# Performance work log

Hardware: AMD Instinct MI355X
Metric: run time of the kernel (lower is better)

## Reference

```python
import jax, jax.numpy as jnp
import numpy as np

EPS = 1e-12


def setup_inputs() -> dict:
    key = jax.random.key(0)
    n, k, Eu, iterations = 200_000, 7, 1_600_000, 3
    k1, k2, k3 = jax.random.split(key, 3)
    # undirected edge list; each undirected edge yields two directed edges
    su = jax.random.randint(k1, (Eu,), 0, n, dtype=jnp.int32)
    du = jax.random.randint(k2, (Eu,), 0, n, dtype=jnp.int32)
    src = jnp.concatenate([su, du])                                   # [E]
    dst = jnp.concatenate([du, su])                                   # [E]
    rev = jnp.concatenate([jnp.arange(Eu, 2 * Eu, dtype=jnp.int32),
                           jnp.arange(Eu, dtype=jnp.int32)])          # [E]
    # node priors (rows sum to 1), mimicking the soft label priors
    prior = jax.random.uniform(k3, (n, k), minval=0.1, maxval=1.0)
    prior = prior / prior.sum(axis=1, keepdims=True)
    # label-to-label potential: log(beta) on the diagonal (beta = 3.0)
    W = jnp.log(3.0) * jnp.eye(k, dtype=jnp.float32)
    return {"prior": prior, "W": W, "src": src, "dst": dst,
            "rev": rev, "iterations": iterations}


def reference(prior, W, src, dst, rev, iterations):
    n, k = prior.shape
    E = src.shape[0]
    psi = jnp.exp(jnp.clip(W, -10.0, 10.0))                           # [k,k]
    msgs = jnp.full((E, k), 1.0 / k, dtype=prior.dtype)

    def step(msgs, _):
        # product of incoming messages per node, in log-space (msgs >= EPS)
        logm = jnp.log(msgs)                                          # [E,k]
        logP = jax.ops.segment_sum(logm, dst, num_segments=n)         # [n,k]
        # per directed edge (i -> j): remove reverse message j -> i
        prod_in_i = jnp.exp(logP[src] - logm[rev])                    # [E,k]
        b = jnp.maximum(prior[src] * prod_in_i, EPS)                  # [E,k]
        m_new = jnp.maximum(b @ psi, EPS)                             # [E,k]
        m_new = m_new / jnp.maximum(m_new.sum(-1, keepdims=True), EPS)
        return m_new, None

    msgs, _ = jax.lax.scan(step, msgs, None, length=int(iterations))

    # beliefs
    logP = jax.ops.segment_sum(jnp.log(msgs), dst, num_segments=n)    # [n,k]
    b = jnp.maximum(prior * jnp.exp(logP), EPS)
    return b / jnp.maximum(b.sum(-1, keepdims=True), EPS)
```

## Files before the change

kernel.cpp:

```cpp
#include <hip/hip_runtime.h>
#include <hip/hip_bf16.h>

#define K 7
#define EPSF 1e-12f
#define LOG_INV_K (-1.9459101090932196f)
#define LOG7 1.9459101090932196f
#define NEG_LOG_EPS 27.631021f
#define SBN 512
#define SBSH 9
#define NSBMAX 768
#define PB 256

#define QSB 409.59375f
#define QSO 2047.96875f
#define QIB (160.0f / 65535.0f)
#define QIO (32.0f / 65535.0f)

__device__ __forceinline__ float ldf(const void* p, size_t idx, int mode) {
    return mode ? ((const float*)p)[idx]
                : __bfloat162float(((const __hip_bfloat16*)p)[idx]);
}

__device__ __forceinline__ void load_psi(const void* W, float* psi, int mode) {
    if (threadIdx.x < K * K) {
        float w = ldf(W, threadIdx.x, mode);
        w = fminf(fmaxf(w, -10.f), 10.f);
        psi[threadIdx.x] = __expf(w);
    }
    __syncthreads();
}

__device__ __forceinline__ void bp_lin(const float* b, const float* psi, float* m) {
    float o[K], sum = 0.f;
#pragma unroll
    for (int j = 0; j < K; j++) {
        float acc = 0.f;
#pragma unroll
        for (int i = 0; i < K; i++) acc += b[i] * psi[i * K + j];
        o[j] = fmaxf(acc, EPSF);
        sum += o[j];
    }
    float inv = __fdividef(1.f, fmaxf(sum, EPSF));
#pragma unroll
    for (int j = 0; j < K; j++) m[j] = o[j] * inv;
}

__device__ __forceinline__ void acc_log_msg(const float* b, const float* psi, float* acc) {
    float m[K];
    bp_lin(b, psi, m);
#pragma unroll
    for (int j = 0; j < K; j++) acc[j] += __logf(m[j]);
}

__device__ __forceinline__ void ld8(const float* base, float* r) {
    const float4* p = (const float4*)base;
    float4 a = p[0], b = p[1];
    r[0]=a.x; r[1]=a.y; r[2]=a.z; r[3]=a.w; r[4]=b.x; r[5]=b.y; r[6]=b.z; r[7]=b.w;
}

__device__ __forceinline__ void dec_pd(uint4 w, float* p, int* degv, int* u1) {
    p[0] = __uint_as_float((w.x & 0xffffu) << 16);
    p[1] = __uint_as_float(w.x & 0xffff0000u);
    p[2] = __uint_as_float((w.y & 0xffffu) << 16);
    p[3] = __uint_as_float(w.y & 0xffff0000u);
    p[4] = __uint_as_float((w.z & 0xffffu) << 16);
    p[5] = __uint_as_float(w.z & 0xffff0000u);
    p[6] = __uint_as_float((w.w & 0xffffu) << 16);
    *degv = (int)((w.w >> 16) & 0x7fffu);
    *u1 = (int)(w.w >> 31);
}

__device__ __forceinline__ uint4 enc_log7(const float* le) {
    float mx = le[0];
#pragma unroll
    for (int i = 1; i < K; i++) mx = fmaxf(mx, le[i]);
    float nb = fminf(fmaxf(-mx, 0.f), 159.9f);
    unsigned qb = (unsigned)(nb * QSB + 0.5f);
    unsigned qo[K];
#pragma unroll
    for (int i = 0; i < K; i++)
        qo[i] = (unsigned)(fminf(mx - le[i], 31.98f) * QSO + 0.5f);
    uint4 r;
    r.x = qb | (qo[0] << 16);
    r.y = qo[1] | (qo[2] << 16);
    r.z = qo[3] | (qo[4] << 16);
    r.w = qo[5] | (qo[6] << 16);
    return r;
}

__device__ __forceinline__ void dec_exp7(uint4 w, float* e) {
    float base = (float)(w.x & 0xffffu) * QIB;
    float o[K];
    o[0] = (float)(w.x >> 16) * QIO;
    o[1] = (float)(w.y & 0xffffu) * QIO;
    o[2] = (float)(w.y >> 16) * QIO;
    o[3] = (float)(w.z & 0xffffu) * QIO;
    o[4] = (float)(w.z >> 16) * QIO;
    o[5] = (float)(w.w & 0xffffu) * QIO;
    o[6] = (float)(w.w >> 16) * QIO;
#pragma unroll
    for (int i = 0; i < K; i++) e[i] = __expf(-(base + o[i]));
}

__global__ void sniff8_kernel(const void* __restrict__ W, int* __restrict__ prm) {
    if (blockIdx.x != 0 || threadIdx.x != 0) return;
    const unsigned int* Wraw = (const unsigned int*)W;
    int mode = ((Wraw[0] >> 16) != 0u) ? 1 : 0;
    float diag0 = 0.f, offd0 = 0.f;
    int structured = 1;
    for (int i = 0; i < K; i++)
        for (int j = 0; j < K; j++) {
            float w = ldf(W, i * K + j, mode);
            w = fminf(fmaxf(w, -10.f), 10.f);
            float e = __expf(w);
            if (i == 0 && j == 0) diag0 = e;
            if (i == 0 && j == 1) offd0 = e;
            if (i == j) { if (i > 0 && e != diag0) structured = 0; }
            else       { if (!(i == 0 && j == 1) && e != offd0) structured = 0; }
        }
    if (!(offd0 >= 0.2f) || !(diag0 >= offd0)) structured = 0;
    prm[0] = mode | (structured << 1);
    ((float*)prm)[1] = offd0;
    ((float*)prm)[2] = diag0;
}

__global__ void hist6_kernel(const int* __restrict__ dst, int* __restrict__ hist,
                             int* __restrict__ btot, int E, int EPB, int NSB) {
    __shared__ int h[NSBMAX];
    for (int i = threadIdx.x; i < NSB; i += 256) h[i] = 0;
    __syncthreads();
    int blk = blockIdx.x;
    int e0 = blk * EPB, e1 = min(e0 + EPB, E);
    for (int e = e0 + (int)threadIdx.x; e < e1; e += 256)
        atomicAdd(&h[dst[e] >> SBSH], 1);
    __syncthreads();
    for (int i = threadIdx.x; i < NSB; i += 256) {
        int c = h[i];
        hist[i * PB + blk] = c;
        if (c) atomicAdd(&btot[i], c);
    }
}

__global__ void bscan6_kernel(const int* __restrict__ btot, int* __restrict__ boff, int NSB) {
    __shared__ int s[1024];
    int t = threadIdx.x;
    int x = (t < NSB) ? btot[t] : 0;
    s[t] = x;
    __syncthreads();
    for (int o = 1; o < 1024; o <<= 1) {
        int y = (t >= o) ? s[t - o] : 0;
        __syncthreads();
        s[t] += y;
        __syncthreads();
    }
    if (t < NSB) boff[t] = s[t] - x;
    if (t == NSB - 1) boff[NSB] = s[t];
}

__global__ void sscan6_kernel(const int* __restrict__ hist, const int* __restrict__ boff,
                              int* __restrict__ woff) {
    __shared__ int s[PB];
    int b = blockIdx.x, t = threadIdx.x;
    int x = hist[b * PB + t];
    s[t] = x;
    __syncthreads();
    for (int o = 1; o < PB; o <<= 1) {
        int y = (t >= o) ? s[t - o] : 0;
        __syncthreads();
        s[t] += y;
        __syncthreads();
    }
    woff[b * PB + t] = boff[b] + s[t] - x;
}

__global__ void part6_kernel(const int* __restrict__ src, const int* __restrict__ dst,
                             const int* __restrict__ woff, unsigned int* __restrict__ coarse,
                             int E, int EPB, int NSB) {
    __shared__ int cur[NSBMAX];
    int blk = blockIdx.x;
    for (int i = threadIdx.x; i < NSB; i += 256) cur[i] = woff[i * PB + blk];
    __syncthreads();
    int e0 = blk * EPB, e1 = min(e0 + EPB, E);
    for (int e = e0 + (int)threadIdx.x; e < e1; e += 256) {
        int d = dst[e];
        int b = d >> SBSH;
        unsigned int pk = (unsigned int)src[e] | ((unsigned int)(d & (SBN - 1)) << 18);
        int pos = atomicAdd(&cur[b], 1);
        coarse[pos] = pk;
    }
}

__global__ void cfill9_kernel(const unsigned int* __restrict__ coarse,
                              const int* __restrict__ boff,
                              const void* __restrict__ prior, const int* __restrict__ prm,
                              int* __restrict__ cur, int* __restrict__ nbr,
                              uint4* __restrict__ PD, int n) {
    __shared__ int lcnt[SBN], lcur[SBN];
    int b = blockIdx.x, t = threadIdx.x;
    int mode = prm[0] & 1;
    for (int i = t; i < SBN; i += 256) lcnt[i] = 0;
    __syncthreads();
    int s0 = boff[b], s1 = boff[b + 1];
    for (int i = s0 + t; i < s1; i += 256)
        atomicAdd(&lcnt[coarse[i] >> 18], 1);
    __syncthreads();
    if (t == 0) {
        int a = s0;
        for (int l = 0; l < SBN; l++) { lcur[l] = a; a += lcnt[l]; }
    }
    __syncthreads();
    int v0 = b << SBSH;
    for (int i = t; i < SBN; i += 256) {
        int v = v0 + i;
        if (v >= n) continue;
        int degv = lcnt[i];
        cur[v] = lcur[i] + degv;
        unsigned int pb[K];
        float p[K];
        if (mode == 0) {
            const unsigned short* pr = (const unsigned short*)prior;
#pragma unroll
            for (int j = 0; j < K; j++) {
                pb[j] = pr[(size_t)v * K + j];
                p[j] = __uint_as_float(pb[j] << 16);
            }
        } else {
            const float* pr = (const float*)prior;
#pragma unroll
            for (int j = 0; j < K; j++) {
                p[j] = pr[(size_t)v * K + j];
                __hip_bfloat16 hh = __float2bfloat16(p[j]);
                pb[j] = *(unsigned short*)&hh;
            }
        }
        float es = __expf((float)(degv - 1) * LOG_INV_K);
        float mx = p[0];
#pragma unroll
        for (int j = 1; j < K; j++) mx = fmaxf(mx, p[j]);
        unsigned int u1 = (mx * es <= EPSF) ? 1u : 0u;
        int dcap = degv > 0x7fff ? 0x7fff : degv;
        uint4 w;
        w.x = pb[0] | (pb[1] << 16);
        w.y = pb[2] | (pb[3] << 16);
        w.z = pb[4] | (pb[5] << 16);
        w.w = pb[6] | (((unsigned int)dcap) << 16) | (u1 << 31);
        PD[v] = w;
    }
    __syncthreads();
    for (int i = s0 + t; i < s1; i += 256) {
        unsigned int w = coarse[i];
        int pos = atomicAdd(&lcur[w >> 18], 1);
        nbr[pos] = (int)(w & 0x3FFFFu);
    }
}

__global__ void n2v9_kernel(const int* __restrict__ cur, const int* __restrict__ nbr,
                            const uint4* __restrict__ PD, const void* __restrict__ W,
                            const int* __restrict__ prm, uint4* __restrict__ LP1,
                            float* __restrict__ EP1f, int n) {
    __shared__ float psi[K * K];
    int pm = prm[0];
    int mode = pm & 1, strq = (pm >> 1) & 1;
    float offd = ((const float*)prm)[1], diag = ((const float*)prm)[2];
    load_psi(W, psi, mode);
    int t = blockIdx.x * blockDim.x + threadIdx.x;
    int v = t >> 2, qi = t & 3;
    if (v >= n) return;
    int start = v ? cur[v - 1] : 0, end = cur[v];
    int len = end - start;
    int lo = start + ((len * qi) >> 2), hi = start + ((len * (qi + 1)) >> 2);
    float cb = diag - offd;
    float acc[K];
    int cn = 0;
    if (strq) {
#pragma unroll
        for (int i = 0; i < K; i++) acc[i] = 1.f;
        for (int e = lo; e < hi; e++) {
            int u = nbr[e];
            uint4 w = PD[u];
            if (w.w >> 31) continue;
            float p[K]; int degu, uu;
            dec_pd(w, p, &degu, &uu);
            float es = __expf((float)(degu - 1) * LOG_INV_K);
            float b[K], S = 0.f;
#pragma unroll
            for (int i = 0; i < K; i++) { b[i] = fmaxf(p[i] * es, EPSF); S += b[i]; }
            float crS = __fdividef(cb, S);
#pragma unroll
            for (int i = 0; i < K; i++) acc[i] *= fmaf(crS, b[i], offd);
            cn++;
        }
#pragma unroll
        for (int i = 0; i < K; i++) {
            acc[i] *= __shfl_xor(acc[i], 1, 64);
            acc[i] *= __shfl_xor(acc[i], 2, 64);
        }
    } else {
#pragma unroll
        for (int i = 0; i < K; i++) acc[i] = 0.f;
        for (int e = lo; e < hi; e++) {
            int u = nbr[e];
            float p[K]; int degu, uu;
            dec_pd(PD[u], p, &degu, &uu);
            float es = __expf((float)(degu - 1) * LOG_INV_K);
            float b[K];
#pragma unroll
            for (int i = 0; i < K; i++) b[i] = fmaxf(p[i] * es, EPSF);
            acc_log_msg(b, psi, acc);
        }
#pragma unroll
        for (int i = 0; i < K; i++) {
            acc[i] += __shfl_xor(acc[i], 1, 64);
            acc[i] += __shfl_xor(acc[i], 2, 64);
        }
    }
    cn += __shfl_xor(cn, 1, 64);
    cn += __shfl_xor(cn, 2, 64);
    if (qi) return;
    float pv[K]; int dv, u1v;
    dec_pd(PD[v], pv, &dv, &u1v);
    float le[K];
    if (strq) {
        float corr = (float)cn * __logf(6.f * offd + diag) + (float)(len - cn) * LOG7;
#pragma unroll
        for (int i = 0; i < K; i++) le[i] = __logf(pv[i] * acc[i]) - corr;
    } else {
#pragma unroll
        for (int i = 0; i < K; i++) le[i] = __logf(pv[i]) + acc[i];
    }
    LP1[v] = enc_log7(le);
    float4* q = (float4*)(EP1f + (size_t)v * 8);
    q[0] = make_float4(__expf(le[0]), __expf(le[1]), __expf(le[2]), __expf(le[3]));
    q[1] = make_float4(__expf(le[4]), __expf(le[5]), __expf(le[6]), 0.f);
}

__global__ void n3v9_kernel(const int* __restrict__ cur, const int* __restrict__ nbr,
                            const uint4* __restrict__ PD, const uint4* __restrict__ LP1,
                            const void* __restrict__ W, const int* __restrict__ prm,
                            uint4* __restrict__ Q2, int n) {
    __shared__ float psi[K * K];
    int pm = prm[0];
    int mode = pm & 1, strq = (pm >> 1) & 1;
    float offd = ((const float*)prm)[1], diag = ((const float*)prm)[2];
    load_psi(W, psi, mode);
    int t = blockIdx.x * blockDim.x + threadIdx.x;
    int v = t >> 2, qi = t & 3;
    if (v >= n) return;
    int start = v ? cur[v - 1] : 0, end = cur[v];
    int len = end - start;
    int lo = start + ((len * qi) >> 2), hi = start + ((len * (qi + 1)) >> 2);
    float cb = diag - offd, norm = 6.f * offd + diag;
    uint4 pdv = PD[v];
    float pv[K]; int dv, u1v;
    dec_pd(pdv, pv, &dv, &u1v);
    float rm1v[K], mrv = 0.f;
    if (strq && u1v) {
#pragma unroll
        for (int i = 0; i < K; i++) rm1v[i] = 7.f;
        mrv = 7.f;
    } else {
        float es = __expf((float)(dv - 1) * LOG_INV_K);
        float b1[K], S1 = 0.f;
#pragma unroll
        for (int i = 0; i < K; i++) { b1[i] = fmaxf(pv[i] * es, EPSF); S1 += b1[i]; }
        if (strq) {
            float inv = __fdividef(1.f, S1 * norm);
#pragma unroll
            for (int i = 0; i < K; i++) {
                float m1 = (offd * S1 + cb * b1[i]) * inv;
                rm1v[i] = __fdividef(1.f, m1);
                mrv = fmaxf(mrv, rm1v[i]);
            }
        } else {
            float m1[K];
            bp_lin(b1, psi, m1);
#pragma unroll
            for (int i = 0; i < K; i++) rm1v[i] = __fdividef(1.f, m1[i]);
        }
    }
    float acc[K];
    int cn = 0;
    if (strq) {
        int tqv = (int)((__logf(mrv) + NEG_LOG_EPS) * QSB) + 1;
#pragma unroll
        for (int i = 0; i < K; i++) acc[i] = 1.f;
        for (int e = lo; e < hi; e++) {
            int u = nbr[e];
            uint4 q = LP1[u];
            if ((int)(q.x & 0xffffu) >= tqv) continue;
            float eu[K];
            dec_exp7(q, eu);
            float b[K], S = 0.f;
#pragma unroll
            for (int i = 0; i < K; i++) { b[i] = fmaxf(eu[i] * rm1v[i], EPSF); S += b[i]; }
            float crS = __fdividef(cb, S);
#pragma unroll
            for (int i = 0; i < K; i++) acc[i] *= fmaf(crS, b[i], offd);
            cn++;
        }
#pragma unroll
        for (int i = 0; i < K; i++) {
            acc[i] *= __shfl_xor(acc[i], 1, 64);
            acc[i] *= __shfl_xor(acc[i], 2, 64);
        }
    } else {
#pragma unroll
        for (int i = 0; i < K; i++) acc[i] = 0.f;
        for (int e = lo; e < hi; e++) {
            int u = nbr[e];
            float eu[K];
            dec_exp7(LP1[u], eu);
            float b[K];
#pragma unroll
            for (int i = 0; i < K; i++) b[i] = fmaxf(eu[i] * rm1v[i], EPSF);
            acc_log_msg(b, psi, acc);
        }
#pragma unroll
        for (int i = 0; i < K; i++) {
            acc[i] += __shfl_xor(acc[i], 1, 64);
            acc[i] += __shfl_xor(acc[i], 2, 64);
        }
    }
    cn += __shfl_xor(cn, 1, 64);
    cn += __shfl_xor(cn, 2, 64);
    if (qi) return;
    float le2[K];
    if (strq) {
        float corr = (float)cn * __logf(norm) + (float)(len - cn) * LOG7;
#pragma unroll
        for (int i = 0; i < K; i++) le2[i] = __logf(pv[i] * acc[i]) - corr;
    } else {
#pragma unroll
        for (int i = 0; i < K; i++) le2[i] = __logf(pv[i]) + acc[i];
    }
    Q2[v] = enc_log7(le2);
}

__global__ void n4v9_kernel(const int* __restrict__ cur, const int* __restrict__ nbr,
                            const uint4* __restrict__ PD, const uint4* __restrict__ Q2,
                            const float* __restrict__ EP1f, const void* __restrict__ prior,
                            const void* __restrict__ W, const int* __restrict__ prm,
                            void* __restrict__ out, int n) {
    __shared__ float psi[K * K];
    int pm = prm[0];
    int mode = pm & 1, strq = (pm >> 1) & 1;
    float offd = ((const float*)prm)[1], diag = ((const float*)prm)[2];
    load_psi(W, psi, mode);
    int t = blockIdx.x * blockDim.x + threadIdx.x;
    int v = t >> 2, qi = t & 3;
    if (v >= n) return;
    int start = v ? cur[v - 1] : 0, end = cur[v];
    int len = end - start;
    int lo = start + ((len * qi) >> 2), hi = start + ((len * (qi + 1)) >> 2);
    float cb = diag - offd, norm = 6.f * offd + diag;
    float e1v[8];
    ld8(EP1f + (size_t)v * 8, e1v);
    float acc[K];
    int cn = 0;
    if (strq) {
        float mx1 = e1v[0];
#pragma unroll
        for (int i = 1; i < K; i++) mx1 = fmaxf(mx1, e1v[i]);
        float F = __fdividef(norm, offd) * 1.01f;
        int m2u = (F * mx1 <= EPSF);
        int tq2c = (int)((LOG7 + NEG_LOG_EPS) * QSB) + 1;
        int tq3  = (int)((__logf(F) + NEG_LOG_EPS) * QSB) + 1;
#pragma unroll
        for (int i = 0; i < K; i++) acc[i] = 1.f;
        if (m2u) {
            for (int e = lo; e < hi; e++) {
                int u = nbr[e];
                uint4 q = Q2[u];
                if ((int)(q.x & 0xffffu) >= tq2c) continue;
                float e2[K];
                dec_exp7(q, e2);
                float b3[K], S = 0.f;
#pragma unroll
                for (int i = 0; i < K; i++) { b3[i] = fmaxf(7.f * e2[i], EPSF); S += b3[i]; }
                float crS = __fdividef(cb, S);
#pragma unroll
                for (int i = 0; i < K; i++) acc[i] *= fmaf(crS, b3[i], offd);
                cn++;
            }
        } else {
            for (int e = lo; e < hi; e++) {
                int u = nbr[e];
                uint4 q = Q2[u];
                if ((int)(q.x & 0xffffu) >= tq3) continue;
                uint4 pdu = PD[u];
                float pu[K]; int degu, u1u;
                dec_pd(pdu, pu, &degu, &u1u);
                float rm1u[K];
                if (u1u) {
#pragma unroll
                    for (int i = 0; i < K; i++) rm1u[i] = 7.f;
                } else {
                    float es = __expf((float)(degu - 1) * LOG_INV_K);
                    float b1[K], S1 = 0.f;
#pragma unroll
                    for (int i = 0; i < K; i++) { b1[i] = fmaxf(pu[i] * es, EPSF); S1 += b1[i]; }
                    float inv = __fdividef(1.f, S1 * norm);
#pragma unroll
                    for (int i = 0; i < K; i++)
                        rm1u[i] = __fdividef(1.f, (offd * S1 + cb * b1[i]) * inv);
                }
                float b2[K], S2 = 0.f;
#pragma unroll
                for (int i = 0; i < K; i++) { b2[i] = fmaxf(e1v[i] * rm1u[i], EPSF); S2 += b2[i]; }
                float inv2 = __fdividef(1.f, S2 * norm);
                float e2[K];
                dec_exp7(q, e2);
                float b3[K], S3 = 0.f;
#pragma unroll
                for (int i = 0; i < K; i++) {
                    float m2 = (offd * S2 + cb * b2[i]) * inv2;
                    b3[i] = fmaxf(__fdividef(e2[i], m2), EPSF);
                    S3 += b3[i];
                }
                float crS3 = __fdividef(cb, S3);
#pragma unroll
                for (int i = 0; i < K; i++) acc[i] *= fmaf(crS3, b3[i], offd);
                cn++;
            }
        }
#pragma unroll
        for (int i = 0; i < K; i++) {
            acc[i] *= __shfl_xor(acc[i], 1, 64);
            acc[i] *= __shfl_xor(acc[i], 2, 64);
        }
    } else {
#pragma unroll
        for (int i = 0; i < K; i++) acc[i] = 0.f;
        for (int e = lo; e < hi; e++) {
            int u = nbr[e];
            uint4 q = Q2[u];
            uint4 pdu = PD[u];
            float pu[K]; int degu, u1u;
            dec_pd(pdu, pu, &degu, &u1u);
            float es = __expf((float)(degu - 1) * LOG_INV_K);
            float b1[K], m1u[K];
#pragma unroll
            for (int i = 0; i < K; i++) b1[i] = fmaxf(pu[i] * es, EPSF);
            bp_lin(b1, psi, m1u);
            float b2[K], m2[K];
#pragma unroll
            for (int i = 0; i < K; i++) b2[i] = fmaxf(__fdividef(e1v[i], m1u[i]), EPSF);
            bp_lin(b2, psi, m2);
            float e2[K];
            dec_exp7(q, e2);
            float b3[K];
#pragma unroll
            for (int i = 0; i < K; i++) b3[i] = fmaxf(__fdividef(e2[i], m2[i]), EPSF);
            acc_log_msg(b3, psi, acc);
        }
#pragma unroll
        for (int i = 0; i < K; i++) {
            acc[i] += __shfl_xor(acc[i], 1, 64);
            acc[i] += __shfl_xor(acc[i], 2, 64);
        }
    }
    cn += __shfl_xor(cn, 1, 64);
    cn += __shfl_xor(cn, 2, 64);
    if (qi) return;
    float bb[K], sum = 0.f;
    if (strq) {
        float corr = (float)cn * __logf(norm) + (float)(len - cn) * LOG7;
#pragma unroll
        for (int i = 0; i < K; i++) {
            float p = ldf(prior, (size_t)v * K + i, mode);
            bb[i] = fmaxf(__expf(__logf(p * acc[i]) - corr), EPSF);
            sum += bb[i];
        }
    } else {
#pragma unroll
        for (int i = 0; i < K; i++) {
            float p = ldf(prior, (size_t)v * K + i, mode);
            bb[i] = fmaxf(p * __expf(acc[i]), EPSF);
            sum += bb[i];
        }
    }
    float inv = __fdividef(1.f, fmaxf(sum, EPSF));
#pragma unroll
    for (int i = 0; i < K; i++) {
        float val = bb[i] * inv;
        if (mode) ((float*)out)[(size_t)v * K + i] = val;
        else ((__hip_bfloat16*)out)[(size_t)v * K + i] = __float2bfloat16(val);
    }
}

__device__ __forceinline__ void bp_msg(const float* b, const float* psi, float* lm) {
    float m[K];
    bp_lin(b, psi, m);
#pragma unroll
    for (int j = 0; j < K; j++) lm[j] = __logf(m[j]);
}
__device__ __forceinline__ void msg1(const void* prior, int node, int degv, int mode,
                                     const float* psi, float* lm) {
    float es = __expf((float)(degv - 1) * LOG_INV_K);
    float b[K];
#pragma unroll
    for (int i = 0; i < K; i++)
        b[i] = fmaxf(ldf(prior, (size_t)node * K + i, mode) * es, EPSF);
    bp_msg(b, psi, lm);
}
__device__ __forceinline__ void msgF(const void* prior, int node,
                                     const float* __restrict__ logP,
                                     const float* lmrev, int mode,
                                     const float* psi, float* lm) {
    float b[K];
#pragma unroll
    for (int i = 0; i < K; i++)
        b[i] = fmaxf(ldf(prior, (size_t)node * K + i, mode) *
                     __expf(logP[(size_t)node * K + i] - lmrev[i]), EPSF);
    bp_msg(b, psi, lm);
}
__global__ void deg_kernel(const int* __restrict__ su, const int* __restrict__ du,
                           int* __restrict__ deg, int Eu) {
    int u = blockIdx.x * blockDim.x + threadIdx.x;
    if (u >= Eu) return;
    atomicAdd(&deg[su[u]], 1);
    atomicAdd(&deg[du[u]], 1);
}
__global__ void pass1_kernel(const int* __restrict__ su, const int* __restrict__ du,
                             const int* __restrict__ deg, const void* __restrict__ prior,
                             const void* __restrict__ W, const int* __restrict__ prm,
                             float* __restrict__ logP1, int Eu) {
    __shared__ float psi[K * K];
    int mode = prm[0] & 1;
    load_psi(W, psi, mode);
    int u = blockIdx.x * blockDim.x + threadIdx.x;
    if (u >= Eu) return;
    int s = su[u], d = du[u];
    float lm[K];
    msg1(prior, s, deg[s], mode, psi, lm);
#pragma unroll
    for (int j = 0; j < K; j++) atomicAdd(&logP1[(size_t)d * K + j], lm[j]);
    msg1(prior, d, deg[d], mode, psi, lm);
#pragma unroll
    for (int j = 0; j < K; j++) atomicAdd(&logP1[(size_t)s * K + j], lm[j]);
}
__global__ void pass2_kernel(const int* __restrict__ su, const int* __restrict__ du,
                             const int* __restrict__ deg, const void* __restrict__ prior,
                             const void* __restrict__ W, const int* __restrict__ prm,
                             const float* __restrict__ logP1, float* __restrict__ logP2, int Eu) {
    __shared__ float psi[K * K];
    int mode = prm[0] & 1;
    load_psi(W, psi, mode);
    int u = blockIdx.x * blockDim.x + threadIdx.x;
    if (u >= Eu) return;
    int s = su[u], d = du[u];
    float lm1sd[K], lm1ds[K], lm[K];
    msg1(prior, s, deg[s], mode, psi, lm1sd);
    msg1(prior, d, deg[d], mode, psi, lm1ds);
    msgF(prior, s, logP1, lm1ds, mode, psi, lm);
#pragma unroll
    for (int j = 0; j < K; j++) atomicAdd(&logP2[(size_t)d * K + j], lm[j]);
    msgF(prior, d, logP1, lm1sd, mode, psi, lm);
#pragma unroll
    for (int j = 0; j < K; j++) atomicAdd(&logP2[(size_t)s * K + j], lm[j]);
}
__global__ void pass3_kernel(const int* __restrict__ su, const int* __restrict__ du,
                             const int* __restrict__ deg, const void* __restrict__ prior,
                             const void* __restrict__ W, const int* __restrict__ prm,
                             const float* __restrict__ logP1, const float* __restrict__ logP2,
                             float* __restrict__ logP3, int Eu) {
    __shared__ float psi[K * K];
    int mode = prm[0] & 1;
    load_psi(W, psi, mode);
    int u = blockIdx.x * blockDim.x + threadIdx.x;
    if (u >= Eu) return;
    int s = su[u], d = du[u];
    float lm1sd[K], lm1ds[K], lm2sd[K], lm2ds[K], lm[K];
    msg1(prior, s, deg[s], mode, psi, lm1sd);
    msg1(prior, d, deg[d], mode, psi, lm1ds);
    msgF(prior, s, logP1, lm1ds, mode, psi, lm2sd);
    msgF(prior, d, logP1, lm1sd, mode, psi, lm2ds);
    msgF(prior, s, logP2, lm2ds, mode, psi, lm);
#pragma unroll
    for (int j = 0; j < K; j++) atomicAdd(&logP3[(size_t)d * K + j], lm[j]);
    msgF(prior, d, logP2, lm2sd, mode, psi, lm);
#pragma unroll
    for (int j = 0; j < K; j++) atomicAdd(&logP3[(size_t)s * K + j], lm[j]);
}
__global__ void belief_kernel(const float* __restrict__ logP3, const void* __restrict__ prior,
                              const int* __restrict__ prm, void* __restrict__ out, int n) {
    int v = blockIdx.x * blockDim.x + threadIdx.x;
    if (v >= n) return;
    int mode = prm[0] & 1;
    float b[K], sum = 0.f;
#pragma unroll
    for (int j = 0; j < K; j++) {
        b[j] = fmaxf(ldf(prior, (size_t)v * K + j, mode) * __expf(logP3[(size_t)v * K + j]), EPSF);
        sum += b[j];
    }
    float inv = __fdividef(1.f, fmaxf(sum, EPSF));
#pragma unroll
    for (int j = 0; j < K; j++) {
        float val = b[j] * inv;
        if (mode) ((float*)out)[(size_t)v * K + j] = val;
        else ((__hip_bfloat16*)out)[(size_t)v * K + j] = __float2bfloat16(val);
    }
}

extern "C" void kernel_launch(void* const* d_in, const int* in_sizes, int n_in,
                              void* d_out, int out_size, void* d_ws, size_t ws_size,
                              hipStream_t stream) {
    const void* prior = d_in[0];
    const void* W     = d_in[1];
    const int* src = (const int*)d_in[2];
    const int* dst = (const int*)d_in[3];

    int n  = in_sizes[0] / K;
    int E  = in_sizes[2];
    int Eu = E / 2;

    const int B = 256;
    int gn  = (n + B - 1) / B;
    int gn4 = (4 * n + B - 1) / B;
    int ge  = (Eu + B - 1) / B;

    int NSB = (n + SBN - 1) >> SBSH;
    int EPB = (E + PB - 1) / PB;

    char* ws = (char*)d_ws;
    size_t off = 0;
    auto alloc = [&](size_t bytes) { size_t o = off; off = (off + bytes + 127) & ~(size_t)127; return o; };

    size_t xsz = (size_t)E * 4;
    if ((size_t)n * 32 > xsz) xsz = (size_t)n * 32;
    size_t o_nbr  = alloc((size_t)E * 4);
    size_t o_X    = alloc(xsz);
    size_t o_PD   = alloc((size_t)n * 16);
    size_t o_EP1f = alloc((size_t)n * 32);
    size_t o_cur  = alloc((size_t)n * 4);
    size_t o_hist = alloc((size_t)NSB * PB * 4);
    size_t o_woff = alloc((size_t)NSB * PB * 4);
    size_t o_boff = alloc((size_t)(NSB + 1) * 4);
    size_t o_btot = alloc((size_t)NSB * 4);
    size_t o_prm  = alloc(64);
    size_t need_v9 = off;

    bool v9_ok = (ws_size >= need_v9) && (n <= (1 << 18)) && (NSB <= NSBMAX) && (NSB >= 1);

    if (v9_ok) {
        int*   nbr    = (int*)(ws + o_nbr);
        unsigned int* coarse = (unsigned int*)(ws + o_X);
        uint4* LP1    = (uint4*)(ws + o_X);
        uint4* Q2     = (uint4*)(ws + o_X + (size_t)n * 16);
        uint4* PD     = (uint4*)(ws + o_PD);
        float* EP1f   = (float*)(ws + o_EP1f);
        int*   cur    = (int*)(ws + o_cur);
        int*   hist   = (int*)(ws + o_hist);
        int*   woff   = (int*)(ws + o_woff);
        int*   boff   = (int*)(ws + o_boff);
        int*   btot   = (int*)(ws + o_btot);
        int*   prm    = (int*)(ws + o_prm);

        sniff8_kernel<<<1, 64, 0, stream>>>(W, prm);
        hipMemsetAsync(btot, 0, (size_t)NSB * 4, stream);
        hist6_kernel<<<PB, B, 0, stream>>>(dst, hist, btot, E, EPB, NSB);
        bscan6_kernel<<<1, 1024, 0, stream>>>(btot, boff, NSB);
        sscan6_kernel<<<NSB, PB, 0, stream>>>(hist, boff, woff);
        part6_kernel<<<PB, B, 0, stream>>>(src, dst, woff, coarse, E, EPB, NSB);
        cfill9_kernel<<<NSB, B, 0, stream>>>(coarse, boff, prior, prm, cur, nbr, PD, n);
        n2v9_kernel<<<gn4, B, 0, stream>>>(cur, nbr, PD, W, prm, LP1, EP1f, n);
        n3v9_kernel<<<gn4, B, 0, stream>>>(cur, nbr, PD, LP1, W, prm, Q2, n);
        n4v9_kernel<<<gn4, B, 0, stream>>>(cur, nbr, PD, Q2, EP1f, prior, W, prm, d_out, n);
        return;
    }

    {
        float* logP1 = (float*)d_ws;
        float* logP2 = logP1 + (size_t)n * K;
        float* logP3 = logP2 + (size_t)n * K;
        int*   deg   = (int*)(logP3 + (size_t)n * K);
        int*   prm   = deg + n;
        sniff8_kernel<<<1, 64, 0, stream>>>(W, prm);
        hipMemsetAsync(d_ws, 0, ((size_t)3 * n * K + n) * sizeof(float), stream);
        deg_kernel<<<ge, B, 0, stream>>>(src, dst, deg, Eu);
        pass1_kernel<<<ge, B, 0, stream>>>(src, dst, deg, prior, W, prm, logP1, Eu);
        pass2_kernel<<<ge, B, 0, stream>>>(src, dst, deg, prior, W, prm, logP1, logP2, Eu);
        pass3_kernel<<<ge, B, 0, stream>>>(src, dst, deg, prior, W, prm, logP1, logP2, logP3, Eu);
        belief_kernel<<<gn, B, 0, stream>>>(logP3, prior, prm, d_out, n);
    }
}
```

Baseline: 325.0 us.

## Precompute per-node first-round messages and switch log quantization to fp16 mantissa-exponent packing

Adds a per-node pass that computes each node's first-round outgoing message once and stores it as packed fp16 in an interleaved buffer. The second pass then just multiplies gathered messages instead of recomputing beliefs per edge, and the last pass reuses those stored messages instead of re-decoding priors. The custom log-domain 16-bit quantization is replaced by fp16 mantissas with a shared power-of-two exponent, which avoids per-element exp in decoding. Edge loops are unrolled by two to overlap the gathers. The costs are an extra kernel launch and some precision loss from fp16 messages. The second pass now always uses the structured-potential product path and drops its general-potential branch.

```diff
diff --git a/kernel.cpp b/kernel.cpp
--- a/kernel.cpp
+++ b/kernel.cpp
@@ -1,20 +1,18 @@
 #include <hip/hip_runtime.h>
 #include <hip/hip_bf16.h>
+#include <hip/hip_fp16.h>
 
 #define K 7
 #define EPSF 1e-12f
 #define LOG_INV_K (-1.9459101090932196f)
 #define LOG7 1.9459101090932196f
-#define NEG_LOG_EPS 27.631021f
+#define LOG2_EPS (-39.8631371f)
+#define LN2 0.69314718056f
+#define INV_LN2 1.44269504f
 #define SBN 512
 #define SBSH 9
 #define NSBMAX 768
 #define PB 256
-
-#define QSB 409.59375f
-#define QSO 2047.96875f
-#define QIB (160.0f / 65535.0f)
-#define QIO (32.0f / 65535.0f)
 
 __device__ __forceinline__ float ldf(const void* p, size_t idx, int mode) {
     return mode ? ((const float*)p)[idx]
@@ -70,36 +68,32 @@
     *u1 = (int)(w.w >> 31);
 }
 
-__device__ __forceinline__ uint4 enc_log7(const float* le) {
-    float mx = le[0];
-#pragma unroll
-    for (int i = 1; i < K; i++) mx = fmaxf(mx, le[i]);
-    float nb = fminf(fmaxf(-mx, 0.f), 159.9f);
-    unsigned qb = (unsigned)(nb * QSB + 0.5f);
-    unsigned qo[K];
-#pragma unroll
-    for (int i = 0; i < K; i++)
-        qo[i] = (unsigned)(fminf(mx - le[i], 31.98f) * QSO + 0.5f);
+__device__ __forceinline__ unsigned short f2h(float f) {
+    __half h = __float2half_rn(f);
+    return *reinterpret_cast<unsigned short*>(&h);
+}
+__device__ __forceinline__ float h2f(unsigned short u) {
+    __half h;
+    *reinterpret_cast<unsigned short*>(&h) = u;
+    return __half2float(h);
+}
+__device__ __forceinline__ uint4 pack7h(const float* m, int E) {
     uint4 r;
-    r.x = qb | (qo[0] << 16);
-    r.y = qo[1] | (qo[2] << 16);
-    r.z = qo[3] | (qo[4] << 16);
-    r.w = qo[5] | (qo[6] << 16);
+    r.x = (unsigned)f2h(m[0]) | ((unsigned)f2h(m[1]) << 16);
+    r.y = (unsigned)f2h(m[2]) | ((unsigned)f2h(m[3]) << 16);
+    r.z = (unsigned)f2h(m[4]) | ((unsigned)f2h(m[5]) << 16);
+    r.w = (unsigned)f2h(m[6]) | ((unsigned)(E & 0xffff) << 16);
     return r;
 }
-
-__device__ __forceinline__ void dec_exp7(uint4 w, float* e) {
-    float base = (float)(w.x & 0xffffu) * QIB;
-    float o[K];
-    o[0] = (float)(w.x >> 16) * QIO;
-    o[1] = (float)(w.y & 0xffffu) * QIO;
-    o[2] = (float)(w.y >> 16) * QIO;
-    o[3] = (float)(w.z & 0xffffu) * QIO;
-    o[4] = (float)(w.z >> 16) * QIO;
-    o[5] = (float)(w.w & 0xffffu) * QIO;
-    o[6] = (float)(w.w >> 16) * QIO;
-#pragma unroll
-    for (int i = 0; i < K; i++) e[i] = __expf(-(base + o[i]));
+__device__ __forceinline__ int unpack7h(uint4 w, float* m) {
+    m[0] = h2f((unsigned short)(w.x & 0xffffu));
+    m[1] = h2f((unsigned short)(w.x >> 16));
+    m[2] = h2f((unsigned short)(w.y & 0xffffu));
+    m[3] = h2f((unsigned short)(w.y >> 16));
+    m[4] = h2f((unsigned short)(w.z & 0xffffu));
+    m[5] = h2f((unsigned short)(w.z >> 16));
+    m[6] = h2f((unsigned short)(w.w & 0xffffu));
+    return (int)(short)(w.w >> 16);
 }
 
 __global__ void sniff8_kernel(const void* __restrict__ W, int* __restrict__ prm) {
@@ -254,90 +248,93 @@
     }
 }
 
-__global__ void n2v9_kernel(const int* __restrict__ cur, const int* __restrict__ nbr,
-                            const uint4* __restrict__ PD, const void* __restrict__ W,
-                            const int* __restrict__ prm, uint4* __restrict__ LP1,
-                            float* __restrict__ EP1f, int n) {
+__global__ void mbuild10_kernel(const uint4* __restrict__ PD, const void* __restrict__ W,
+                                const int* __restrict__ prm, uint4* __restrict__ R32, int n) {
     __shared__ float psi[K * K];
     int pm = prm[0];
     int mode = pm & 1, strq = (pm >> 1) & 1;
     float offd = ((const float*)prm)[1], diag = ((const float*)prm)[2];
     load_psi(W, psi, mode);
+    int v = blockIdx.x * blockDim.x + threadIdx.x;
+    if (v >= n) return;
+    float p[K]; int dv, u1v;
+    dec_pd(PD[v], p, &dv, &u1v);
+    float es = __expf((float)(dv - 1) * LOG_INV_K);
+    float b[K], S = 0.f;
+#pragma unroll
+    for (int i = 0; i < K; i++) { b[i] = fmaxf(p[i] * es, EPSF); S += b[i]; }
+    float m1n[K];
+    if (strq) {
+        float cb = diag - offd, norm = 6.f * offd + diag;
+        float sc = __fdividef(7.f, S * norm);
+#pragma unroll
+        for (int i = 0; i < K; i++) m1n[i] = (offd * S + cb * b[i]) * sc;
+    } else {
+        float m1[K];
+        bp_lin(b, psi, m1);
+#pragma unroll
+        for (int i = 0; i < K; i++) m1n[i] = 7.f * m1[i];
+    }
+    R32[2 * (size_t)v] = pack7h(m1n, 0);
+}
+
+__global__ void n2v10_kernel(const int* __restrict__ cur, const int* __restrict__ nbr,
+                             const uint4* __restrict__ R32, const uint4* __restrict__ PD,
+                             const int* __restrict__ prm, uint4* __restrict__ LP1,
+                             float* __restrict__ EP1f, int n) {
     int t = blockIdx.x * blockDim.x + threadIdx.x;
     int v = t >> 2, qi = t & 3;
     if (v >= n) return;
     int start = v ? cur[v - 1] : 0, end = cur[v];
     int len = end - start;
     int lo = start + ((len * qi) >> 2), hi = start + ((len * (qi + 1)) >> 2);
-    float cb = diag - offd;
-    float acc[K];
-    int cn = 0;
-    if (strq) {
-#pragma unroll
-        for (int i = 0; i < K; i++) acc[i] = 1.f;
-        for (int e = lo; e < hi; e++) {
-            int u = nbr[e];
-            uint4 w = PD[u];
-            if (w.w >> 31) continue;
-            float p[K]; int degu, uu;
-            dec_pd(w, p, &degu, &uu);
-            float es = __expf((float)(degu - 1) * LOG_INV_K);
-            float b[K], S = 0.f;
-#pragma unroll
-            for (int i = 0; i < K; i++) { b[i] = fmaxf(p[i] * es, EPSF); S += b[i]; }
-            float crS = __fdividef(cb, S);
-#pragma unroll
-            for (int i = 0; i < K; i++) acc[i] *= fmaf(crS, b[i], offd);
-            cn++;
-        }
-#pragma unroll
-        for (int i = 0; i < K; i++) {
-            acc[i] *= __shfl_xor(acc[i], 1, 64);
-            acc[i] *= __shfl_xor(acc[i], 2, 64);
-        }
-    } else {
-#pragma unroll
-        for (int i = 0; i < K; i++) acc[i] = 0.f;
-        for (int e = lo; e < hi; e++) {
-            int u = nbr[e];
-            float p[K]; int degu, uu;
-            dec_pd(PD[u], p, &degu, &uu);
-            float es = __expf((float)(degu - 1) * LOG_INV_K);
-            float b[K];
-#pragma unroll
-            for (int i = 0; i < K; i++) b[i] = fmaxf(p[i] * es, EPSF);
-            acc_log_msg(b, psi, acc);
-        }
-#pragma unroll
-        for (int i = 0; i < K; i++) {
-            acc[i] += __shfl_xor(acc[i], 1, 64);
-            acc[i] += __shfl_xor(acc[i], 2, 64);
-        }
-    }
-    cn += __shfl_xor(cn, 1, 64);
-    cn += __shfl_xor(cn, 2, 64);
+    float acc[K] = {1.f, 1.f, 1.f, 1.f, 1.f, 1.f, 1.f};
+    int e = lo;
+    for (; e + 1 < hi; e += 2) {
+        int ua = nbr[e], ub = nbr[e + 1];
+        uint4 wa = R32[2 * (size_t)ua];
+        uint4 wb = R32[2 * (size_t)ub];
+        float a[K], c[K];
+        unpack7h(wa, a);
+        unpack7h(wb, c);
+#pragma unroll
+        for (int i = 0; i < K; i++) acc[i] *= a[i] * c[i];
+    }
+    if (e < hi) {
+        float a[K];
+        unpack7h(R32[2 * (size_t)nbr[e]], a);
+#pragma unroll
+        for (int i = 0; i < K; i++) acc[i] *= a[i];
+    }
+#pragma unroll
+    for (int i = 0; i < K; i++) {
+        acc[i] *= __shfl_xor(acc[i], 1, 64);
+        acc[i] *= __shfl_xor(acc[i], 2, 64);
+    }
     if (qi) return;
     float pv[K]; int dv, u1v;
     dec_pd(PD[v], pv, &dv, &u1v);
-    float le[K];
-    if (strq) {
-        float corr = (float)cn * __logf(6.f * offd + diag) + (float)(len - cn) * LOG7;
-#pragma unroll
-        for (int i = 0; i < K; i++) le[i] = __logf(pv[i] * acc[i]) - corr;
-    } else {
-#pragma unroll
-        for (int i = 0; i < K; i++) le[i] = __logf(pv[i]) + acc[i];
-    }
-    LP1[v] = enc_log7(le);
+    float le[K], mx = -1e30f;
+    float corr = (float)len * LOG7;
+#pragma unroll
+    for (int i = 0; i < K; i++) {
+        le[i] = __logf(pv[i] * acc[i]) - corr;
+        mx = fmaxf(mx, le[i]);
+    }
+    int E1 = (int)ceilf(mx * INV_LN2);
+    float fm[K];
+#pragma unroll
+    for (int i = 0; i < K; i++) fm[i] = __expf(le[i] - (float)E1 * LN2);
+    LP1[v] = pack7h(fm, E1);
     float4* q = (float4*)(EP1f + (size_t)v * 8);
-    q[0] = make_float4(__expf(le[0]), __expf(le[1]), __expf(le[2]), __expf(le[3]));
-    q[1] = make_float4(__expf(le[4]), __expf(le[5]), __expf(le[6]), 0.f);
-}
-
-__global__ void n3v9_kernel(const int* __restrict__ cur, const int* __restrict__ nbr,
-                            const uint4* __restrict__ PD, const uint4* __restrict__ LP1,
-                            const void* __restrict__ W, const int* __restrict__ prm,
-                            uint4* __restrict__ Q2, int n) {
+    q[0] = make_float4(ldexpf(fm[0], E1), ldexpf(fm[1], E1), ldexpf(fm[2], E1), ldexpf(fm[3], E1));
+    q[1] = make_float4(ldexpf(fm[4], E1), ldexpf(fm[5], E1), ldexpf(fm[6], E1), 0.f);
+}
+
+__global__ void n3v10_kernel(const int* __restrict__ cur, const int* __restrict__ nbr,
+                             const uint4* __restrict__ PD, const uint4* __restrict__ LP1,
+                             const void* __restrict__ W, const int* __restrict__ prm,
+                             uint4* __restrict__ R32, int n) {
     __shared__ float psi[K * K];
     int pm = prm[0];
     int mode = pm & 1, strq = (pm >> 1) & 1;
@@ -350,9 +347,8 @@
     int len = end - start;
     int lo = start + ((len * qi) >> 2), hi = start + ((len * (qi + 1)) >> 2);
     float cb = diag - offd, norm = 6.f * offd + diag;
-    uint4 pdv = PD[v];
     float pv[K]; int dv, u1v;
-    dec_pd(pdv, pv, &dv, &u1v);
+    dec_pd(PD[v], pv, &dv, &u1v);
     float rm1v[K], mrv = 0.f;
     if (strq && u1v) {
 #pragma unroll
@@ -381,23 +377,32 @@
     float acc[K];
     int cn = 0;
     if (strq) {
-        int tqv = (int)((__logf(mrv) + NEG_LOG_EPS) * QSB) + 1;
+        int Ethr = (int)floorf(LOG2_EPS - log2f(mrv));
 #pragma unroll
         for (int i = 0; i < K; i++) acc[i] = 1.f;
-        for (int e = lo; e < hi; e++) {
-            int u = nbr[e];
-            uint4 q = LP1[u];
-            if ((int)(q.x & 0xffffu) >= tqv) continue;
-            float eu[K];
-            dec_exp7(q, eu);
+        auto proc = [&](uint4 q) {
+            float m[K];
+            int E = unpack7h(q, m);
+            if (E <= Ethr) return;
             float b[K], S = 0.f;
 #pragma unroll
-            for (int i = 0; i < K; i++) { b[i] = fmaxf(eu[i] * rm1v[i], EPSF); S += b[i]; }
+            for (int i = 0; i < K; i++) {
+                b[i] = fmaxf(ldexpf(m[i] * rm1v[i], E), EPSF);
+                S += b[i];
+            }
             float crS = __fdividef(cb, S);
 #pragma unroll
             for (int i = 0; i < K; i++) acc[i] *= fmaf(crS, b[i], offd);
             cn++;
-        }
+        };
+        int e = lo;
+        for (; e + 1 < hi; e += 2) {
+            int ua = nbr[e], ub = nbr[e + 1];
+            uint4 qa = LP1[ua], qb = LP1[ub];
+            proc(qa);
+            proc(qb);
+        }
+        if (e < hi) proc(LP1[nbr[e]]);
 #pragma unroll
         for (int i = 0; i < K; i++) {
             acc[i] *= __shfl_xor(acc[i], 1, 64);
@@ -407,12 +412,12 @@
 #pragma unroll
         for (int i = 0; i < K; i++) acc[i] = 0.f;
         for (int e = lo; e < hi; e++) {
-            int u = nbr[e];
-            float eu[K];
-            dec_exp7(LP1[u], eu);
+            float m[K];
+            int E = unpack7h(LP1[nbr[e]], m);
             float b[K];
 #pragma unroll
-            for (int i = 0; i < K; i++) b[i] = fmaxf(eu[i] * rm1v[i], EPSF);
+            for (int i = 0; i < K; i++)
+                b[i] = fmaxf(ldexpf(m[i] * rm1v[i], E), EPSF);
             acc_log_msg(b, psi, acc);
         }
 #pragma unroll
@@ -424,23 +429,32 @@
     cn += __shfl_xor(cn, 1, 64);
     cn += __shfl_xor(cn, 2, 64);
     if (qi) return;
-    float le2[K];
+    float le2[K], mx = -1e30f;
     if (strq) {
         float corr = (float)cn * __logf(norm) + (float)(len - cn) * LOG7;
 #pragma unroll
-        for (int i = 0; i < K; i++) le2[i] = __logf(pv[i] * acc[i]) - corr;
+        for (int i = 0; i < K; i++) {
+            le2[i] = __logf(pv[i] * acc[i]) - corr;
+            mx = fmaxf(mx, le2[i]);
+        }
     } else {
 #pragma unroll
-        for (int i = 0; i < K; i++) le2[i] = __logf(pv[i]) + acc[i];
-    }
-    Q2[v] = enc_log7(le2);
-}
-
-__global__ void n4v9_kernel(const int* __restrict__ cur, const int* __restrict__ nbr,
-                            const uint4* __restrict__ PD, const uint4* __restrict__ Q2,
-                            const float* __restrict__ EP1f, const void* __restrict__ prior,
-                            const void* __restrict__ W, const int* __restrict__ prm,
-                            void* __restrict__ out, int n) {
+        for (int i = 0; i < K; i++) {
+            le2[i] = __logf(pv[i]) + acc[i];
+            mx = fmaxf(mx, le2[i]);
+        }
+    }
+    int E2 = (int)ceilf(mx * INV_LN2);
+    float fm[K];
+#pragma unroll
+    for (int i = 0; i < K; i++) fm[i] = __expf(le2[i] - (float)E2 * LN2);
+    R32[2 * (size_t)v + 1] = pack7h(fm, E2);
+}
+
+__global__ void n4v10_kernel(const int* __restrict__ cur, const int* __restrict__ nbr,
+                             const uint4* __restrict__ R32, const float* __restrict__ EP1f,
+                             const void* __restrict__ prior, const void* __restrict__ W,
+                             const int* __restrict__ prm, void* __restrict__ out, int n) {
     __shared__ float psi[K * K];
     int pm = prm[0];
     int mode = pm & 1, strq = (pm >> 1) & 1;
@@ -463,58 +477,57 @@
         for (int i = 1; i < K; i++) mx1 = fmaxf(mx1, e1v[i]);
         float F = __fdividef(norm, offd) * 1.01f;
         int m2u = (F * mx1 <= EPSF);
-        int tq2c = (int)((LOG7 + NEG_LOG_EPS) * QSB) + 1;
-        int tq3  = (int)((__logf(F) + NEG_LOG_EPS) * QSB) + 1;
+        int Ethr2 = (int)floorf(LOG2_EPS - log2f(7.f));
+        int Ethr3 = (int)floorf(LOG2_EPS - log2f(F));
 #pragma unroll
         for (int i = 0; i < K; i++) acc[i] = 1.f;
         if (m2u) {
-            for (int e = lo; e < hi; e++) {
-                int u = nbr[e];
-                uint4 q = Q2[u];
-                if ((int)(q.x & 0xffffu) >= tq2c) continue;
-                float e2[K];
-                dec_exp7(q, e2);
+            auto proc = [&](uint4 q) {
+                float m[K];
+                int E2 = unpack7h(q, m);
+                if (E2 <= Ethr2) return;
                 float b3[K], S = 0.f;
 #pragma unroll
-                for (int i = 0; i < K; i++) { b3[i] = fmaxf(7.f * e2[i], EPSF); S += b3[i]; }
+                for (int i = 0; i < K; i++) {
+                    b3[i] = fmaxf(ldexpf(m[i] * 7.f, E2), EPSF);
+                    S += b3[i];
+                }
                 float crS = __fdividef(cb, S);
 #pragma unroll
                 for (int i = 0; i < K; i++) acc[i] *= fmaf(crS, b3[i], offd);
                 cn++;
+            };
+            int e = lo;
+            for (; e + 1 < hi; e += 2) {
+                int ua = nbr[e], ub = nbr[e + 1];
+                uint4 qa = R32[2 * (size_t)ua + 1];
+                uint4 qb = R32[2 * (size_t)ub + 1];
+                proc(qa);
+                proc(qb);
             }
+            if (e < hi) proc(R32[2 * (size_t)nbr[e] + 1]);
         } else {
             for (int e = lo; e < hi; e++) {
-                int u = nbr[e];
-                uint4 q = Q2[u];
-                if ((int)(q.x & 0xffffu) >= tq3) continue;
-                uint4 pdu = PD[u];
-                float pu[K]; int degu, u1u;
-                dec_pd(pdu, pu, &degu, &u1u);
-                float rm1u[K];
-                if (u1u) {
-#pragma unroll
-                    for (int i = 0; i < K; i++) rm1u[i] = 7.f;
-                } else {
-                    float es = __expf((float)(degu - 1) * LOG_INV_K);
-                    float b1[K], S1 = 0.f;
-#pragma unroll
-                    for (int i = 0; i < K; i++) { b1[i] = fmaxf(pu[i] * es, EPSF); S1 += b1[i]; }
-                    float inv = __fdividef(1.f, S1 * norm);
-#pragma unroll
-                    for (int i = 0; i < K; i++)
-                        rm1u[i] = __fdividef(1.f, (offd * S1 + cb * b1[i]) * inv);
+                size_t u = (size_t)nbr[e];
+                uint4 q = R32[2 * u + 1];
+                float m[K];
+                int E2 = unpack7h(q, m);
+                if (E2 <= Ethr3) continue;
+                float tt[K];
+                unpack7h(R32[2 * u], tt);
+                float b2[K], S2 = 0.f;
+#pragma unroll
+                for (int i = 0; i < K; i++) {
+                    b2[i] = fmaxf(e1v[i] * __fdividef(7.f, tt[i]), EPSF);
+                    S2 += b2[i];
                 }
-                float b2[K], S2 = 0.f;
-#pragma unroll
-                for (int i = 0; i < K; i++) { b2[i] = fmaxf(e1v[i] * rm1u[i], EPSF); S2 += b2[i]; }
                 float inv2 = __fdividef(1.f, S2 * norm);
-                float e2[K];
-                dec_exp7(q, e2);
                 float b3[K], S3 = 0.f;
 #pragma unroll
                 for (int i = 0; i < K; i++) {
-                    float m2 = (offd * S2 + cb * b2[i]) * inv2;
-                    b3[i] = fmaxf(__fdividef(e2[i], m2), EPSF);
+                    float m2v = (offd * S2 + cb * b2[i]) * inv2;
+                    float e2 = ldexpf(m[i], E2);
+                    b3[i] = fmaxf(__fdividef(e2, m2v), EPSF);
                     S3 += b3[i];
                 }
                 float crS3 = __fdividef(cb, S3);
@@ -532,25 +545,24 @@
 #pragma unroll
         for (int i = 0; i < K; i++) acc[i] = 0.f;
         for (int e = lo; e < hi; e++) {
-            int u = nbr[e];
-            uint4 q = Q2[u];
-            uint4 pdu = PD[u];
-            float pu[K]; int degu, u1u;
-            dec_pd(pdu, pu, &degu, &u1u);
-            float es = __expf((float)(degu - 1) * LOG_INV_K);
-            float b1[K], m1u[K];
-#pragma unroll
-            for (int i = 0; i < K; i++) b1[i] = fmaxf(pu[i] * es, EPSF);
-            bp_lin(b1, psi, m1u);
-            float b2[K], m2[K];
-#pragma unroll
-            for (int i = 0; i < K; i++) b2[i] = fmaxf(__fdividef(e1v[i], m1u[i]), EPSF);
+            size_t u = (size_t)nbr[e];
+            uint4 q = R32[2 * u + 1];
+            float m[K];
+            int E2 = unpack7h(q, m);
+            float tt[K];
+            unpack7h(R32[2 * u], tt);
+            float b2[K];
+#pragma unroll
+            for (int i = 0; i < K; i++)
+                b2[i] = fmaxf(e1v[i] * __fdividef(7.f, tt[i]), EPSF);
+            float m2[K];
             bp_lin(b2, psi, m2);
-            float e2[K];
-            dec_exp7(q, e2);
             float b3[K];
 #pragma unroll
-            for (int i = 0; i < K; i++) b3[i] = fmaxf(__fdividef(e2[i], m2[i]), EPSF);
+            for (int i = 0; i < K; i++) {
+                float e2 = ldexpf(m[i], E2);
+                b3[i] = fmaxf(__fdividef(e2, m2[i]), EPSF);
+            }
             acc_log_msg(b3, psi, acc);
         }
 #pragma unroll
@@ -727,7 +739,7 @@
     auto alloc = [&](size_t bytes) { size_t o = off; off = (off + bytes + 127) & ~(size_t)127; return o; };
 
     size_t xsz = (size_t)E * 4;
-    if ((size_t)n * 32 > xsz) xsz = (size_t)n * 32;
+    if ((size_t)n * 48 > xsz) xsz = (size_t)n * 48;
     size_t o_nbr  = alloc((size_t)E * 4);
     size_t o_X    = alloc(xsz);
     size_t o_PD   = alloc((size_t)n * 16);
@@ -738,15 +750,15 @@
     size_t o_boff = alloc((size_t)(NSB + 1) * 4);
     size_t o_btot = alloc((size_t)NSB * 4);
     size_t o_prm  = alloc(64);
-    size_t need_v9 = off;
-
-    bool v9_ok = (ws_size >= need_v9) && (n <= (1 << 18)) && (NSB <= NSBMAX) && (NSB >= 1);
-
-    if (v9_ok) {
+    size_t need_v10 = off;
+
+    bool v10_ok = (ws_size >= need_v10) && (n <= (1 << 18)) && (NSB <= NSBMAX) && (NSB >= 1);
+
+    if (v10_ok) {
         int*   nbr    = (int*)(ws + o_nbr);
         unsigned int* coarse = (unsigned int*)(ws + o_X);
         uint4* LP1    = (uint4*)(ws + o_X);
-        uint4* Q2     = (uint4*)(ws + o_X + (size_t)n * 16);
+        uint4* R32    = (uint4*)(ws + o_X + (size_t)n * 16);
         uint4* PD     = (uint4*)(ws + o_PD);
         float* EP1f   = (float*)(ws + o_EP1f);
         int*   cur    = (int*)(ws + o_cur);
@@ -763,9 +775,10 @@
         sscan6_kernel<<<NSB, PB, 0, stream>>>(hist, boff, woff);
         part6_kernel<<<PB, B, 0, stream>>>(src, dst, woff, coarse, E, EPB, NSB);
         cfill9_kernel<<<NSB, B, 0, stream>>>(coarse, boff, prior, prm, cur, nbr, PD, n);
-        n2v9_kernel<<<gn4, B, 0, stream>>>(cur, nbr, PD, W, prm, LP1, EP1f, n);
-        n3v9_kernel<<<gn4, B, 0, stream>>>(cur, nbr, PD, LP1, W, prm, Q2, n);
-        n4v9_kernel<<<gn4, B, 0, stream>>>(cur, nbr, PD, Q2, EP1f, prior, W, prm, d_out, n);
+        mbuild10_kernel<<<gn, B, 0, stream>>>(PD, W, prm, R32, n);
+        n2v10_kernel<<<gn4, B, 0, stream>>>(cur, nbr, R32, PD, prm, LP1, EP1f, n);
+        n3v10_kernel<<<gn4, B, 0, stream>>>(cur, nbr, PD, LP1, W, prm, R32, n);
+        n4v10_kernel<<<gn4, B, 0, stream>>>(cur, nbr, R32, EP1f, prior, W, prm, d_out, n);
         return;
     }
 
```

Result: faster. 318.5 us (-2.0%).
